# Kernel optimization log

Hardware: AMD Instinct MI355X
Metric: run time of the kernel (lower is better)

The kernel has to match this reference:

```python
import jax, jax.numpy as jnp
import numpy as np

N, E, IN, OUT, R, B = 20000, 640000, 128, 128, 64, 16


def setup_inputs() -> dict:
    key = jax.random.key(0)
    ks = jax.random.split(key, 9)
    xav_w = float(np.sqrt(2.0 / (IN + OUT)))  # xavier-uniform-ish scale
    xav_c = float(np.sqrt(2.0 / (R + B)))
    return {
        "x": jax.random.normal(ks[0], (N, IN), jnp.float32),
        "weight": jax.random.normal(ks[1], (B, IN, OUT), jnp.float32) * xav_w,
        "w_comp": jax.random.normal(ks[2], (R, B), jnp.float32) * xav_c,
        "h_bias": jnp.zeros((OUT,), jnp.float32),
        "loop_weight": jax.random.normal(ks[3], (IN, OUT), jnp.float32) * xav_w,
        "norm": jax.random.uniform(ks[4], (E, 1), jnp.float32),
        "src": jax.random.randint(ks[5], (E,), 0, N, jnp.int32),
        "dst": jax.random.randint(ks[6], (E,), 0, N, jnp.int32),
        "etypes": jax.random.randint(ks[7], (E,), 0, R, jnp.int32),
    }


def reference(x, weight, w_comp, h_bias, loop_weight, norm, src, dst, etypes):
    # Basis composition: per-relation weights W_rel[r] = sum_b w_comp[r,b] * weight[b]
    W_rel = jnp.einsum("rb,bio->rio", w_comp, weight)          # [R, IN, OUT]
    # Project every node through every relation weight (N*R << per-edge bmm
    # of E gathered [IN,OUT] matrices; same math as bmm_maybe_select).
    h_all = jnp.einsum("ni,rio->nro", x, W_rel)                 # [N, R, OUT]
    # Per-edge message: msg_e = x[src_e] @ W_rel[etype_e], scaled by norm
    msg = h_all[src, etypes] * norm                              # [E, OUT]
    # fn.sum aggregation to destination nodes
    agg = jax.ops.segment_sum(msg, dst, num_segments=x.shape[0])  # [N, OUT]
    out = agg + h_bias + x @ loop_weight                          # bias + self-loop
    return jax.nn.relu(out)                                       # activation; dropout p=0
```

## Files before the change

### kernel.cpp

```cpp
#include <hip/hip_runtime.h>

#define N_NODES 20000
#define E_EDGES 640000
#define R_REL   64
#define B_BASES 16
#define NSEG    128
#define SEGLEN  (E_EDGES / NSEG)
#define RH      10000
#define NBPR    32
#define QG      ((2 * NSEG) / 16)

typedef __attribute__((ext_vector_type(4))) float f32x4;
typedef __attribute__((ext_vector_type(8))) _Float16 half8;

__device__ inline float h2f(unsigned short v) {
    _Float16 h; __builtin_memcpy(&h, &v, 2); return (float)h;
}
__device__ inline unsigned short f2h(float f) {
    _Float16 h = (_Float16)f; unsigned short v; __builtin_memcpy(&v, &h, 2); return v;
}

__device__ inline void gld_lds16(const void* g, void* l) {
    __builtin_amdgcn_global_load_lds(
        (const __attribute__((address_space(1))) void*)g,
        (__attribute__((address_space(3))) void*)l, 16, 0, 0);
}


__global__ void k_wrelh(const float* weight, const float* w_comp, unsigned short* wt_h,
                        const float* lw, unsigned short* lwT)
{
    __shared__ float tile[32][33];
    __shared__ float wcS[B_BASES];
    int bid = blockIdx.x;
    int tx = threadIdx.x & 31, ty = threadIdx.x >> 5;
    if (bid >= R_REL * 16) {
        int q = bid - R_REL * 16;
        int ti = q >> 2, tj = q & 3;
        const float* srcp = lw + (ti * 32) * 128 + tj * 32;
        #pragma unroll
        for (int s = 0; s < 4; s++)
            tile[ty + s * 8][tx] = srcp[(ty + s * 8) * 128 + tx];
        __syncthreads();
        unsigned short* d = lwT + (tj * 32) * 128 + ti * 32;
        #pragma unroll
        for (int s = 0; s < 4; s++)
            d[(ty + s * 8) * 128 + tx] = f2h(tile[tx][ty + s * 8]);
        return;
    }
    int r  = bid >> 4;
    int ti = (bid >> 2) & 3;
    int tj = bid & 3;
    if (threadIdx.x < B_BASES) wcS[threadIdx.x] = w_comp[r * B_BASES + threadIdx.x];
    __syncthreads();
    float acc[4] = {0.f, 0.f, 0.f, 0.f};
    const float* wp = weight + (ti * 32) * 128 + tj * 32;
    for (int b = 0; b < B_BASES; b++) {
        float c = wcS[b];
        #pragma unroll
        for (int s = 0; s < 4; s++)
            acc[s] += c * wp[b * 16384 + (ty + s * 8) * 128 + tx];
    }
    #pragma unroll
    for (int s = 0; s < 4; s++) tile[ty + s * 8][tx] = acc[s];
    __syncthreads();
    unsigned short* dstp = wt_h + r * 16384 + (tj * 32) * 128 + ti * 32;
    #pragma unroll
    for (int s = 0; s < 4; s++)
        dstp[(ty + s * 8) * 128 + tx] = f2h(tile[tx][ty + s * 8]);
}

__global__ void k_xhalf(const float* x, unsigned short* xh)
{
    int i4 = blockIdx.x * 256 + threadIdx.x;
    float4 v = ((const float4*)x)[i4];
    ushort4 o;
    o.x = f2h(v.x); o.y = f2h(v.y); o.z = f2h(v.z); o.w = f2h(v.w);
    ((ushort4*)xh)[i4] = o;
}

__global__ void k_histp(const int* etypes, const int* dst, int* hp, int* he)
{
    __shared__ int lh[RH];
    __shared__ int heL[R_REL];
    int t = threadIdx.x, q = blockIdx.x;
    int s = q >> 1, h = q & 1;
    for (int i = t; i < RH; i += 256) lh[i] = 0;
    if (t < R_REL) heL[t] = 0;
    __syncthreads();
    int e0 = s * SEGLEN;
    for (int k = t; k < SEGLEN; k += 256) {
        int e = e0 + k;
        int d = dst[e];
        unsigned ld = (unsigned)(d - h * RH);
        if (ld < RH) {
            atomicAdd(&lh[ld], 1);
            atomicAdd(&heL[etypes[e]], 1);
        }
    }
    __syncthreads();
    for (int i = t; i < RH; i += 256) hp[s * N_NODES + h * RH + i] = lh[i];
    if (t < R_REL) he[q * 64 + t] = heL[t];
}

__global__ void k_sumc(const int* hp, int* counts2)
{
    int n = blockIdx.x * 256 + threadIdx.x;
    if (n >= N_NODES) return;
    int s = 0;
    for (int q = 0; q < NSEG; q += 8) {
        int v[8];
        #pragma unroll
        for (int k = 0; k < 8; k++) v[k] = hp[(q + k) * N_NODES + n];
        #pragma unroll
        for (int k = 0; k < 8; k++) s += v[k];
    }
    counts2[n] = s;
}

__global__ void k_scan_all2(const int* he, const int* counts2,
                            int* offsets, int* off2, int* be)
{
    __shared__ int part[1024];
    __shared__ int psum[16][R_REL];
    __shared__ int offL[R_REL];
    int tid = threadIdx.x;
    int t = tid & 63;
    int g = tid >> 6;
    int vals[QG];
    int ps = 0;
    #pragma unroll
    for (int k = 0; k < QG; k++) {
        vals[k] = he[(g * QG + k) * 64 + t];
        ps += vals[k];
    }
    psum[g][t] = ps;
    __syncthreads();
    if (tid < 64) {
        int c = 0;
        #pragma unroll
        for (int gg = 0; gg < 16; gg++) c += psum[gg][t];
        int s1 = c;
        for (int d = 1; d < 64; d <<= 1) {
            int a1 = __shfl_up(s1, d);
            if (t >= d) s1 += a1;
        }
        offsets[t] = s1 - c;
        offL[t] = s1 - c;
        if (t == 63) offsets[64] = s1;
    }
    __syncthreads();
    {
        int run = offL[t];
        for (int gg = 0; gg < g; gg++) run += psum[gg][t];
        #pragma unroll
        for (int k = 0; k < QG; k++) {
            be[(g * QG + k) * 64 + t] = run;
            run += vals[k];
        }
    }
    int lo_i = tid * 20, hi_i = lo_i + 20;
    if (hi_i > N_NODES) hi_i = N_NODES;
    if (lo_i > N_NODES) lo_i = N_NODES;
    int s = 0;
    for (int i = lo_i; i < hi_i; i++) s += counts2[i];
    part[tid] = s;
    __syncthreads();
    for (int d = 1; d < 1024; d <<= 1) {
        int v = (tid >= d) ? part[tid - d] : 0;
        __syncthreads();
        part[tid] += v;
        __syncthreads();
    }
    int run = part[tid] - s;
    for (int i = lo_i; i < hi_i; i++) {
        off2[i] = run;
        run += counts2[i];
    }
    if (tid == 1023) off2[N_NODES] = run;
}

__global__ void k_segbase(const int* off2, int* hp)
{
    int n = blockIdx.x * 256 + threadIdx.x;
    if (n >= N_NODES) return;
    int run = off2[n];
    for (int q = 0; q < NSEG; q += 8) {
        int v[8];
        #pragma unroll
        for (int k = 0; k < 8; k++) v[k] = hp[(q + k) * N_NODES + n];
        #pragma unroll
        for (int k = 0; k < 8; k++) { hp[(q + k) * N_NODES + n] = run; run += v[k]; }
    }
}

__global__ void k_scatter3(const int* etypes, const int* dst, const int* src, const float* norm,
                           const int* hp, const int* be,
                           int* perm_src, float* pnorm, int* pos2)
{
    __shared__ int lbase[RH];
    __shared__ int ebase[R_REL];
    int t = threadIdx.x, q = blockIdx.x;
    int s = q >> 1, h = q & 1;
    for (int i = t; i < RH; i += 256) lbase[i] = hp[s * N_NODES + h * RH + i];
    if (t < R_REL) ebase[t] = be[q * 64 + t];
    __syncthreads();
    int e0 = s * SEGLEN;
    for (int k = t; k < SEGLEN; k += 256) {
        int e = e0 + k;
        int d = dst[e];
        unsigned ld = (unsigned)(d - h * RH);
        if (ld < RH) {
            int slot = atomicAdd(&lbase[ld], 1);
            int p = atomicAdd(&ebase[etypes[e]], 1);
            perm_src[p] = src[e];
            pnorm[p] = norm[e];
            pos2[p] = slot;
        }
    }
}

__global__ __launch_bounds__(256) void k_edge_mfma(
    const unsigned short* __restrict__ xh, const unsigned short* __restrict__ wt_h,
    const int* __restrict__ perm_src, const float* __restrict__ pnorm,
    const int* __restrict__ pos2, const int* __restrict__ offsets,
    unsigned short* __restrict__ msg)
{
    __shared__ __align__(16) char smemW[32768];
    int t = threadIdx.x, b = blockIdx.x;
    int r = b >> 5;
    int j = b & (NBPR - 1);
    int p0 = offsets[r], p1 = offsets[r + 1];
    int nch = (p1 - p0 + 63) >> 6;

    {
        const size_t rbase = (size_t)r * 16384;
        #pragma unroll
        for (int it = 0; it < 8; it++) {
            int s = it * 256 + t;
            int o = s >> 4, ch = s & 15;
            int jx = ch ^ (o & 15);
            gld_lds16(wt_h + rbase + o * 128 + jx * 8, smemW + s * 16);
        }
    }

    int l = t & 63, w = t >> 6;
    int lg = l >> 4, lr = l & 15;
    int rowA = w * 16 + lr;
    const half8* smW = (const half8*)smemW;

    int i = j;
    int sN = 0;
    if (i < nch) {
        int e0 = p0 + i * 64;
        int cnt = p1 - e0; if (cnt > 64) cnt = 64;
        sN = (rowA < cnt) ? perm_src[e0 + rowA] : 0;
    }

    __syncthreads();

    half8 avC[4];
    {
        const half8* xr = (const half8*)(xh + (size_t)sN * 128);
        #pragma unroll
        for (int kk = 0; kk < 4; kk++) avC[kk] = xr[kk * 4 + lg];
    }
    int i2 = i + NBPR;
    if (i2 < nch) {
        int e0 = p0 + i2 * 64;
        int cnt = p1 - e0; if (cnt > 64) cnt = 64;
        sN = (rowA < cnt) ? perm_src[e0 + rowA] : 0;
    }

    while (i < nch) {
        int e0 = p0 + i * 64;
        int cnt = p1 - e0; if (cnt > 64) cnt = 64;

        int slotC[4]; float nrmC[4];
        #pragma unroll
        for (int jj = 0; jj < 4; jj++) {
            int row = w * 16 + lg * 4 + jj;
            bool vld = row < cnt;
            slotC[jj] = vld ? pos2[e0 + row] : -1;
            nrmC[jj]  = vld ? pnorm[e0 + row] : 0.0f;
        }

        half8 avN[4];
        {
            const half8* xr = (const half8*)(xh + (size_t)sN * 128);
            #pragma unroll
            for (int kk = 0; kk < 4; kk++) avN[kk] = xr[kk * 4 + lg];
        }
        int i3 = i2 + NBPR;
        if (i3 < nch) {
            int e0n = p0 + i3 * 64;
            int cntn = p1 - e0n; if (cntn > 64) cntn = 64;
            sN = (rowA < cntn) ? perm_src[e0n + rowA] : 0;
        }

        f32x4 acc[8];
        #pragma unroll
        for (int n = 0; n < 8; n++) acc[n] = {0.0f, 0.0f, 0.0f, 0.0f};

        #pragma unroll
        for (int kk = 0; kk < 4; kk++) {
            #pragma unroll
            for (int n = 0; n < 8; n++) {
                int o = n * 16 + lr;
                half8 bv = smW[o * 16 + ((kk * 4 + lg) ^ (o & 15))];
                acc[n] = __builtin_amdgcn_mfma_f32_16x16x32_f16(avC[kk], bv, acc[n], 0, 0, 0);
            }
        }

        #pragma unroll
        for (int jj = 0; jj < 4; jj++) {
            int slot = slotC[jj];
            if (slot >= 0) {
                float nm = nrmC[jj];
                uint4 ov;
                ov.x = (unsigned int)f2h(acc[0][jj] * nm) | ((unsigned int)f2h(acc[1][jj] * nm) << 16);
                ov.y = (unsigned int)f2h(acc[2][jj] * nm) | ((unsigned int)f2h(acc[3][jj] * nm) << 16);
                ov.z = (unsigned int)f2h(acc[4][jj] * nm) | ((unsigned int)f2h(acc[5][jj] * nm) << 16);
                ov.w = (unsigned int)f2h(acc[6][jj] * nm) | ((unsigned int)f2h(acc[7][jj] * nm) << 16);
                *(uint4*)(msg + (size_t)slot * 128 + lr * 8) = ov;
            }
        }

        #pragma unroll
        for (int kk = 0; kk < 4; kk++) avC[kk] = avN[kk];
        i = i2; i2 = i3;
    }
}

__global__ __launch_bounds__(256) void k_selfmfma(
    const unsigned short* __restrict__ xh, const unsigned short* __restrict__ lwT,
    float* __restrict__ out)
{
    __shared__ __align__(16) char smemW[32768];
    int t = threadIdx.x, b = blockIdx.x;
    int n0 = b * 64;

    #pragma unroll
    for (int it = 0; it < 8; it++) {
        int s = it * 256 + t;
        int o = s >> 4, ch = s & 15;
        int jx = ch ^ (o & 15);
        gld_lds16(lwT + o * 128 + jx * 8, smemW + s * 16);
    }

    int l = t & 63, w = t >> 6;
    int lg = l >> 4, lr = l & 15;
    int rowA = w * 16 + lr;
    int nA = n0 + rowA; if (nA >= N_NODES) nA = N_NODES - 1;
    const half8* xr = (const half8*)(xh + (size_t)nA * 128);
    half8 avC[4];
    #pragma unroll
    for (int kk = 0; kk < 4; kk++) avC[kk] = xr[kk * 4 + lg];

    f32x4 acc[8];
    #pragma unroll
    for (int n = 0; n < 8; n++) acc[n] = {0.0f, 0.0f, 0.0f, 0.0f};

    __syncthreads();

    const half8* smW = (const half8*)smemW;
    #pragma unroll
    for (int kk = 0; kk < 4; kk++) {
        #pragma unroll
        for (int n = 0; n < 8; n++) {
            int o = n * 16 + lr;
            half8 bv = smW[o * 16 + ((kk * 4 + lg) ^ (o & 15))];
            acc[n] = __builtin_amdgcn_mfma_f32_16x16x32_f16(avC[kk], bv, acc[n], 0, 0, 0);
        }
    }

    #pragma unroll
    for (int jj = 0; jj < 4; jj++) {
        int row = w * 16 + lg * 4 + jj;
        int n = n0 + row;
        if (n < N_NODES) {
            float4 v0, v1;
            v0.x = acc[0][jj]; v0.y = acc[1][jj]; v0.z = acc[2][jj]; v0.w = acc[3][jj];
            v1.x = acc[4][jj]; v1.y = acc[5][jj]; v1.z = acc[6][jj]; v1.w = acc[7][jj];
            *(float4*)(out + (size_t)n * 128 + lr * 8) = v0;
            *(float4*)(out + (size_t)n * 128 + lr * 8 + 4) = v1;
        }
    }
}

__global__ void k_msgsum(const unsigned short* msg, const int* off2,
                         const float* bias, float* out)
{
    __shared__ float4 red[256];
    __shared__ float fin[128];
    int n = blockIdx.x, t = threadIdx.x;
    int m0 = off2[n], m1 = off2[n + 1];
    int rp = t >> 5, c = t & 31;
    float4 a; a.x = 0.f; a.y = 0.f; a.z = 0.f; a.w = 0.f;
    for (int j = m0 + rp; j < m1; j += 8) {
        uint2 v = *(const uint2*)(msg + (size_t)j * 128 + c * 4);
        a.x += h2f((unsigned short)(v.x & 0xffff));
        a.y += h2f((unsigned short)(v.x >> 16));
        a.z += h2f((unsigned short)(v.y & 0xffff));
        a.w += h2f((unsigned short)(v.y >> 16));
    }
    red[t] = a;
    __syncthreads();
    if (t < 128) {
        float4 b = red[t + 128];
        red[t].x += b.x; red[t].y += b.y; red[t].z += b.z; red[t].w += b.w;
    }
    __syncthreads();
    if (t < 64) {
        float4 b = red[t + 64];
        red[t].x += b.x; red[t].y += b.y; red[t].z += b.z; red[t].w += b.w;
    }
    __syncthreads();
    if (t < 32) {
        float4 v = red[t], b = red[t + 32];
        v.x += b.x; v.y += b.y; v.z += b.z; v.w += b.w;
        float4 o = *(const float4*)(out + (size_t)n * 128 + t * 4);
        v.x += o.x; v.y += o.y; v.z += o.z; v.w += o.w;
        int base = (t & 1) * 64 + (t >> 1);
        fin[base]      = v.x;
        fin[base + 16] = v.y;
        fin[base + 32] = v.z;
        fin[base + 48] = v.w;
    }
    __syncthreads();
    if (t < 32) {
        float4 f = ((const float4*)fin)[t];
        float4 bb = *(const float4*)(bias + t * 4);
        f.x += bb.x; f.y += bb.y; f.z += bb.z; f.w += bb.w;
        if (f.x < 0.f) f.x = 0.f;
        if (f.y < 0.f) f.y = 0.f;
        if (f.z < 0.f) f.z = 0.f;
        if (f.w < 0.f) f.w = 0.f;
        *(float4*)(out + (size_t)n * 128 + t * 4) = f;
    }
}


__global__ void k_wrel(const float* weight, const float* w_comp, float* W_rel)
{
    int idx = blockIdx.x * 256 + threadIdx.x;
    int r  = idx >> 14;
    int io = idx & 16383;
    float acc = 0.0f;
    for (int b = 0; b < B_BASES; b++)
        acc += w_comp[r * B_BASES + b] * weight[b * 16384 + io];
    W_rel[idx] = acc;
}

__global__ void k_zero(float* agg, int* counts, int* counts2)
{
    int idx = blockIdx.x * 256 + threadIdx.x;
    if (idx < N_NODES * 128) agg[idx] = 0.0f;
    if (idx < R_REL) counts[idx] = 0;
    if (idx < N_NODES) counts2[idx] = 0;
}

__global__ void k_hist(const int* etypes, int* counts)
{
    __shared__ int h[R_REL];
    int t = threadIdx.x;
    if (t < R_REL) h[t] = 0;
    __syncthreads();
    int e = blockIdx.x * 256 + t;
    atomicAdd(&h[etypes[e]], 1);
    __syncthreads();
    if (t < R_REL && h[t] != 0) atomicAdd(&counts[t], h[t]);
}

__global__ void k_scan(const int* counts, int* offsets, int* cursor, int* co)
{
    if (threadIdx.x == 0) {
        int run = 0, c = 0;
        for (int r = 0; r < R_REL; r++) {
            offsets[r] = run; cursor[r] = run; co[r] = c;
            run += counts[r];
            c   += (counts[r] + 63) >> 6;
        }
        offsets[R_REL] = run; co[R_REL] = c;
    }
}

__global__ void k_scatter(const int* etypes, int* cursor, int* perm)
{
    __shared__ int h[R_REL];
    __shared__ int base[R_REL];
    int t = threadIdx.x;
    if (t < R_REL) h[t] = 0;
    __syncthreads();
    int e = blockIdx.x * 256 + t;
    int et = etypes[e];
    int rank = atomicAdd(&h[et], 1);
    __syncthreads();
    if (t < R_REL && h[t] != 0) base[t] = atomicAdd(&cursor[t], h[t]);
    __syncthreads();
    perm[base[et] + rank] = e;
}

__global__ void k_edge_atomic(const float* x, const float* W_rel, const float* norm,
                              const int* src, const int* dst, const int* perm,
                              const int* offsets, const int* co, float* agg)
{
    __shared__ float4 WfS[2048];
    __shared__ float4 xsS[1024];
    __shared__ int coS[R_REL + 1];
    __shared__ int srcS[64], dstS[64];
    __shared__ float normS[64];
    int t = threadIdx.x, bid = blockIdx.x;
    if (t <= R_REL) coS[t] = co[t];
    __syncthreads();
    if (bid >= coS[R_REL]) return;
    int r = 0;
    while (bid >= coS[r + 1]) r++;
    int e0 = offsets[r] + (bid - coS[r]) * 64;
    int cnt = offsets[r + 1] - e0;
    if (cnt > 64) cnt = 64;
    if (t < 64) {
        if (t < cnt) {
            int eid = perm[e0 + t];
            srcS[t] = src[eid]; dstS[t] = dst[eid]; normS[t] = norm[eid];
        } else { srcS[t] = 0; dstS[t] = 0; normS[t] = 0.0f; }
    }
    const float* xsf = (const float*)xsS;
    int q  = t & 31;
    int eb = t >> 5;
    float4 acc[8];
    for (int k = 0; k < 8; k++) { acc[k].x = 0.f; acc[k].y = 0.f; acc[k].z = 0.f; acc[k].w = 0.f; }
    for (int h = 0; h < 2; h++) {
        __syncthreads();
        const float4* Wsrc = (const float4*)(W_rel + r * 16384 + h * 8192);
        for (int p = 0; p < 8; p++) WfS[p * 256 + t] = Wsrc[p * 256 + t];
        for (int p = 0; p < 4; p++) {
            int idx = p * 256 + t;
            int e = idx >> 4, c = idx & 15;
            xsS[idx] = ((const float4*)(x + srcS[e] * 128 + h * 64))[c];
        }
        __syncthreads();
        for (int i = 0; i < 64; i++) {
            float4 wv = WfS[i * 32 + q];
            for (int k = 0; k < 8; k++) {
                float xv = xsf[(eb + 8 * k) * 64 + i];
                acc[k].x += xv * wv.x;
                acc[k].y += xv * wv.y;
                acc[k].z += xv * wv.z;
                acc[k].w += xv * wv.w;
            }
        }
    }
    for (int k = 0; k < 8; k++) {
        int e = eb + 8 * k;
        if (e < cnt) {
            float nrm = normS[e];
            float* row = agg + dstS[e] * 128 + q * 4;
            atomicAdd(row + 0, acc[k].x * nrm);
            atomicAdd(row + 1, acc[k].y * nrm);
            atomicAdd(row + 2, acc[k].z * nrm);
            atomicAdd(row + 3, acc[k].w * nrm);
        }
    }
}

__global__ void k_out(const float* x, const float* loop_w, const float* agg,
                      const float* bias, float* out)
{
    __shared__ float xrow[128];
    int n = blockIdx.x;
    int o = threadIdx.x;
    xrow[o] = x[n * 128 + o];
    __syncthreads();
    float acc = 0.0f;
    for (int i = 0; i < 128; i++)
        acc += xrow[i] * loop_w[i * 128 + o];
    float val = acc + agg[n * 128 + o] + bias[o];
    if (val < 0.0f) val = 0.0f;
    out[n * 128 + o] = val;
}

extern "C" void kernel_launch(void* const* d_in, const int* in_sizes, int n_in,
                              void* d_out, int out_size, void* d_ws, size_t ws_size,
                              hipStream_t stream)
{
    const float* x      = (const float*)d_in[0];
    const float* weight = (const float*)d_in[1];
    const float* w_comp = (const float*)d_in[2];
    const float* h_bias = (const float*)d_in[3];
    const float* loop_w = (const float*)d_in[4];
    const float* norm   = (const float*)d_in[5];
    const int* src    = (const int*)d_in[6];
    const int* dst    = (const int*)d_in[7];
    const int* etypes = (const int*)d_in[8];
    float* out = (float*)d_out;

    char* ws = (char*)d_ws;
    size_t off = 0;
    float* W_rel = (float*)(ws + off); off += (size_t)R_REL * 16384 * 4;
    float* agg   = (float*)(ws + off); off += (size_t)N_NODES * 128 * 4;
    int* perm    = (int*)(ws + off);   off += (size_t)E_EDGES * 4;
    int* counts  = (int*)(ws + off);   off += 64 * 4;
    int* offsets = (int*)(ws + off);   off += 68 * 4;
    int* cursor  = (int*)(ws + off);   off += 64 * 4;
    int* co      = (int*)(ws + off);   off += 68 * 4;
    int* counts2 = (int*)(ws + off);   off += (size_t)N_NODES * 4;
    int* off2    = (int*)(ws + off);   off += (size_t)(N_NODES + 4) * 4;
    int* cursor2 = (int*)(ws + off);   off += (size_t)N_NODES * 4;
    int* pos2    = (int*)(ws + off);   off += (size_t)E_EDGES * 4;
    unsigned short* msg = (unsigned short*)(ws + off);
    size_t need_big = off + (size_t)E_EDGES * 128 * 2;
    int big = (ws_size >= need_big) ? 1 : 0;

    if (big) {
        unsigned short* wt_h = (unsigned short*)W_rel;
        char* wspare = (char*)W_rel + (size_t)2 * 1024 * 1024;
        unsigned short* lwT = (unsigned short*)wspare;
        unsigned short* xh = (unsigned short*)agg;
        float* pnorm = (float*)((char*)agg + (size_t)N_NODES * 128 * 2);
        int* perm_src = perm;
        int* hp = (int*)msg;
        int* he = (int*)((char*)msg + (size_t)NSEG * N_NODES * 4);
        int* be = (int*)((char*)he + (size_t)2 * NSEG * 64 * 4);

        k_wrelh<<<R_REL * 16 + 16, 256, 0, stream>>>(weight, w_comp, wt_h, loop_w, lwT);
        k_xhalf<<<(N_NODES * 128 / 4) / 256, 256, 0, stream>>>(x, xh);
        k_histp<<<2 * NSEG, 256, 0, stream>>>(etypes, dst, hp, he);
        k_sumc<<<(N_NODES + 255) / 256, 256, 0, stream>>>(hp, counts2);
        k_scan_all2<<<1, 1024, 0, stream>>>(he, counts2, offsets, off2, be);
        k_segbase<<<(N_NODES + 255) / 256, 256, 0, stream>>>(off2, hp);
        k_scatter3<<<2 * NSEG, 256, 0, stream>>>(etypes, dst, src, norm,
                                                 hp, be, perm_src, pnorm, pos2);
        k_edge_mfma<<<R_REL * NBPR, 256, 0, stream>>>(
            xh, wt_h, perm_src, pnorm, pos2, offsets, msg);
        k_selfmfma<<<(N_NODES + 63) / 64, 256, 0, stream>>>(xh, lwT, out);
        k_msgsum<<<N_NODES, 256, 0, stream>>>(msg, off2, h_bias, out);
    } else {
        k_wrel<<<(R_REL * 16384) / 256, 256, 0, stream>>>(weight, w_comp, W_rel);
        k_zero<<<(N_NODES * 128) / 256, 256, 0, stream>>>(agg, counts, counts2);
        k_hist<<<E_EDGES / 256, 256, 0, stream>>>(etypes, counts);
        k_scan<<<1, 64, 0, stream>>>(counts, offsets, cursor, co);
        k_scatter<<<E_EDGES / 256, 256, 0, stream>>>(etypes, cursor, perm);
        k_edge_atomic<<<E_EDGES / 64 + R_REL, 256, 0, stream>>>(
            x, W_rel, norm, src, dst, perm, offsets, co, agg);
        k_out<<<N_NODES, 128, 0, stream>>>(x, loop_w, agg, h_bias, out);
    }
}
```

Before: 266.4 us.

## Merge prep kernels, compress per-segment histograms to u16, fuse self-loop into edge kernel

Merges the weight composition, loop-weight transpose, x-to-half conversion and histogram kernels into one launch. Per-segment node histograms are stored as 16-bit values, and k_segbase now computes segment-local prefixes without off2, which k_scatter3 adds back. The self-loop MFMA blocks are appended to the edge-MFMA grid. The intent is fewer launches and less histogram traffic. It relies on a single segment's count per node fitting in 16 bits, and it makes the block roles in the merged grids uneven.

Result: no change. 268.7 us (+0.8%).

```diff
diff --git a/kernel.cpp b/kernel.cpp
--- a/kernel.cpp
+++ b/kernel.cpp
@@ -10,6 +10,13 @@
 #define NBPR    32
 #define QG      ((2 * NSEG) / 16)
 
+#define PB_WREL (R_REL * 16)
+#define PB_LW   (PB_WREL + 16)
+#define PB_XH   (PB_LW + 2500)
+#define PB_HIST (PB_XH + 2 * NSEG)
+
+#define SELF_B  ((N_NODES + 63) / 64)
+
 typedef __attribute__((ext_vector_type(4))) float f32x4;
 typedef __attribute__((ext_vector_type(8))) _Float16 half8;
 
@@ -26,16 +33,44 @@
         (__attribute__((address_space(3))) void*)l, 16, 0, 0);
 }
 
-
-__global__ void k_wrelh(const float* weight, const float* w_comp, unsigned short* wt_h,
-                        const float* lw, unsigned short* lwT)
+__global__ void k_prep(const float* weight, const float* w_comp, unsigned short* wt_h,
+                       const float* lw, unsigned short* lwT,
+                       const float* x, unsigned short* xh,
+                       const int* etypes, const int* dst,
+                       unsigned short* hps, int* he)
 {
     __shared__ float tile[32][33];
     __shared__ float wcS[B_BASES];
-    int bid = blockIdx.x;
-    int tx = threadIdx.x & 31, ty = threadIdx.x >> 5;
-    if (bid >= R_REL * 16) {
-        int q = bid - R_REL * 16;
+    __shared__ int lh[RH];
+    __shared__ int heL[R_REL];
+    int b = blockIdx.x, t = threadIdx.x;
+    int tx = t & 31, ty = t >> 5;
+
+    if (b < PB_WREL) {
+        int r  = b >> 4;
+        int ti = (b >> 2) & 3;
+        int tj = b & 3;
+        if (t < B_BASES) wcS[t] = w_comp[r * B_BASES + t];
+        __syncthreads();
+        float acc[4] = {0.f, 0.f, 0.f, 0.f};
+        const float* wp = weight + (ti * 32) * 128 + tj * 32;
+        for (int bb = 0; bb < B_BASES; bb++) {
+            float c = wcS[bb];
+            #pragma unroll
+            for (int s = 0; s < 4; s++)
+                acc[s] += c * wp[bb * 16384 + (ty + s * 8) * 128 + tx];
+        }
+        #pragma unroll
+        for (int s = 0; s < 4; s++) tile[ty + s * 8][tx] = acc[s];
+        __syncthreads();
+        unsigned short* dstp = wt_h + r * 16384 + (tj * 32) * 128 + ti * 32;
+        #pragma unroll
+        for (int s = 0; s < 4; s++)
+            dstp[(ty + s * 8) * 128 + tx] = f2h(tile[tx][ty + s * 8]);
+        return;
+    }
+    if (b < PB_LW) {
+        int q = b - PB_WREL;
         int ti = q >> 2, tj = q & 3;
         const float* srcp = lw + (ti * 32) * 128 + tj * 32;
         #pragma unroll
@@ -48,62 +83,38 @@
             d[(ty + s * 8) * 128 + tx] = f2h(tile[tx][ty + s * 8]);
         return;
     }
-    int r  = bid >> 4;
-    int ti = (bid >> 2) & 3;
-    int tj = bid & 3;
-    if (threadIdx.x < B_BASES) wcS[threadIdx.x] = w_comp[r * B_BASES + threadIdx.x];
-    __syncthreads();
-    float acc[4] = {0.f, 0.f, 0.f, 0.f};
-    const float* wp = weight + (ti * 32) * 128 + tj * 32;
-    for (int b = 0; b < B_BASES; b++) {
-        float c = wcS[b];
-        #pragma unroll
-        for (int s = 0; s < 4; s++)
-            acc[s] += c * wp[b * 16384 + (ty + s * 8) * 128 + tx];
-    }
-    #pragma unroll
-    for (int s = 0; s < 4; s++) tile[ty + s * 8][tx] = acc[s];
-    __syncthreads();
-    unsigned short* dstp = wt_h + r * 16384 + (tj * 32) * 128 + ti * 32;
-    #pragma unroll
-    for (int s = 0; s < 4; s++)
-        dstp[(ty + s * 8) * 128 + tx] = f2h(tile[tx][ty + s * 8]);
-}
-
-__global__ void k_xhalf(const float* x, unsigned short* xh)
-{
-    int i4 = blockIdx.x * 256 + threadIdx.x;
-    float4 v = ((const float4*)x)[i4];
-    ushort4 o;
-    o.x = f2h(v.x); o.y = f2h(v.y); o.z = f2h(v.z); o.w = f2h(v.w);
-    ((ushort4*)xh)[i4] = o;
-}
-
-__global__ void k_histp(const int* etypes, const int* dst, int* hp, int* he)
-{
-    __shared__ int lh[RH];
-    __shared__ int heL[R_REL];
-    int t = threadIdx.x, q = blockIdx.x;
-    int s = q >> 1, h = q & 1;
-    for (int i = t; i < RH; i += 256) lh[i] = 0;
-    if (t < R_REL) heL[t] = 0;
-    __syncthreads();
-    int e0 = s * SEGLEN;
-    for (int k = t; k < SEGLEN; k += 256) {
-        int e = e0 + k;
-        int d = dst[e];
-        unsigned ld = (unsigned)(d - h * RH);
-        if (ld < RH) {
-            atomicAdd(&lh[ld], 1);
-            atomicAdd(&heL[etypes[e]], 1);
-        }
-    }
-    __syncthreads();
-    for (int i = t; i < RH; i += 256) hp[s * N_NODES + h * RH + i] = lh[i];
-    if (t < R_REL) he[q * 64 + t] = heL[t];
-}
-
-__global__ void k_sumc(const int* hp, int* counts2)
+    if (b < PB_XH) {
+        int i4 = (b - PB_LW) * 256 + t;
+        float4 v = ((const float4*)x)[i4];
+        ushort4 o;
+        o.x = f2h(v.x); o.y = f2h(v.y); o.z = f2h(v.z); o.w = f2h(v.w);
+        ((ushort4*)xh)[i4] = o;
+        return;
+    }
+    {
+        int q = b - PB_XH;
+        int s = q >> 1, h = q & 1;
+        for (int i = t; i < RH; i += 256) lh[i] = 0;
+        if (t < R_REL) heL[t] = 0;
+        __syncthreads();
+        int e0 = s * SEGLEN;
+        for (int k = t; k < SEGLEN; k += 256) {
+            int e = e0 + k;
+            int d = dst[e];
+            unsigned ld = (unsigned)(d - h * RH);
+            if (ld < RH) {
+                atomicAdd(&lh[ld], 1);
+                atomicAdd(&heL[etypes[e]], 1);
+            }
+        }
+        __syncthreads();
+        for (int i = t; i < RH; i += 256)
+            hps[(size_t)s * N_NODES + h * RH + i] = (unsigned short)lh[i];
+        if (t < R_REL) he[q * 64 + t] = heL[t];
+    }
+}
+
+__global__ void k_sumc(const unsigned short* hps, int* counts2)
 {
     int n = blockIdx.x * 256 + threadIdx.x;
     if (n >= N_NODES) return;
@@ -111,11 +122,28 @@
     for (int q = 0; q < NSEG; q += 8) {
         int v[8];
         #pragma unroll
-        for (int k = 0; k < 8; k++) v[k] = hp[(q + k) * N_NODES + n];
+        for (int k = 0; k < 8; k++) v[k] = hps[(size_t)(q + k) * N_NODES + n];
         #pragma unroll
         for (int k = 0; k < 8; k++) s += v[k];
     }
     counts2[n] = s;
+}
+
+__global__ void k_segbase(unsigned short* hps)
+{
+    int n = blockIdx.x * 256 + threadIdx.x;
+    if (n >= N_NODES) return;
+    int run = 0;
+    for (int q = 0; q < NSEG; q += 8) {
+        int v[8];
+        #pragma unroll
+        for (int k = 0; k < 8; k++) v[k] = hps[(size_t)(q + k) * N_NODES + n];
+        #pragma unroll
+        for (int k = 0; k < 8; k++) {
+            hps[(size_t)(q + k) * N_NODES + n] = (unsigned short)run;
+            run += v[k];
+        }
+    }
 }
 
 __global__ void k_scan_all2(const int* he, const int* counts2,
@@ -180,29 +208,16 @@
     if (tid == 1023) off2[N_NODES] = run;
 }
 
-__global__ void k_segbase(const int* off2, int* hp)
-{
-    int n = blockIdx.x * 256 + threadIdx.x;
-    if (n >= N_NODES) return;
-    int run = off2[n];
-    for (int q = 0; q < NSEG; q += 8) {
-        int v[8];
-        #pragma unroll
-        for (int k = 0; k < 8; k++) v[k] = hp[(q + k) * N_NODES + n];
-        #pragma unroll
-        for (int k = 0; k < 8; k++) { hp[(q + k) * N_NODES + n] = run; run += v[k]; }
-    }
-}
-
 __global__ void k_scatter3(const int* etypes, const int* dst, const int* src, const float* norm,
-                           const int* hp, const int* be,
+                           const unsigned short* hps, const int* be, const int* off2,
                            int* perm_src, float* pnorm, int* pos2)
 {
     __shared__ int lbase[RH];
     __shared__ int ebase[R_REL];
     int t = threadIdx.x, q = blockIdx.x;
     int s = q >> 1, h = q & 1;
-    for (int i = t; i < RH; i += 256) lbase[i] = hp[s * N_NODES + h * RH + i];
+    for (int i = t; i < RH; i += 256)
+        lbase[i] = off2[h * RH + i] + (int)hps[(size_t)s * N_NODES + h * RH + i];
     if (t < R_REL) ebase[t] = be[q * 64 + t];
     __syncthreads();
     int e0 = s * SEGLEN;
@@ -222,12 +237,60 @@
 
 __global__ __launch_bounds__(256) void k_edge_mfma(
     const unsigned short* __restrict__ xh, const unsigned short* __restrict__ wt_h,
+    const unsigned short* __restrict__ lwT,
     const int* __restrict__ perm_src, const float* __restrict__ pnorm,
     const int* __restrict__ pos2, const int* __restrict__ offsets,
-    unsigned short* __restrict__ msg)
+    unsigned short* __restrict__ msg, float* __restrict__ out)
 {
     __shared__ __align__(16) char smemW[32768];
     int t = threadIdx.x, b = blockIdx.x;
+    int l = t & 63, w = t >> 6;
+    int lg = l >> 4, lr = l & 15;
+    const half8* smW = (const half8*)smemW;
+
+    if (b >= R_REL * NBPR) {
+        int n0 = (b - R_REL * NBPR) * 64;
+        #pragma unroll
+        for (int it = 0; it < 8; it++) {
+            int s = it * 256 + t;
+            int o = s >> 4, ch = s & 15;
+            int jx = ch ^ (o & 15);
+            gld_lds16(lwT + o * 128 + jx * 8, smemW + s * 16);
+        }
+        int rowA = w * 16 + lr;
+        int nA = n0 + rowA; if (nA >= N_NODES) nA = N_NODES - 1;
+        const half8* xr = (const half8*)(xh + (size_t)nA * 128);
+        half8 avC[4];
+        #pragma unroll
+        for (int kk = 0; kk < 4; kk++) avC[kk] = xr[kk * 4 + lg];
+        f32x4 acc[8];
+        #pragma unroll
+        for (int n = 0; n < 8; n++) acc[n] = {0.0f, 0.0f, 0.0f, 0.0f};
+        __syncthreads();
+        #pragma unroll
+        for (int kk = 0; kk < 4; kk++) {
+            #pragma unroll
+            for (int n = 0; n < 8; n++) {
+                int o = n * 16 + lr;
+                half8 bv = smW[o * 16 + ((kk * 4 + lg) ^ (o & 15))];
+                acc[n] = __builtin_amdgcn_mfma_f32_16x16x32_f16(avC[kk], bv, acc[n], 0, 0, 0);
+            }
+        }
+        #pragma unroll
+        for (int jj = 0; jj < 4; jj++) {
+            int row = w * 16 + lg * 4 + jj;
+            int n = n0 + row;
+            if (n < N_NODES) {
+                float4 v0, v1;
+                v0.x = acc[0][jj]; v0.y = acc[1][jj]; v0.z = acc[2][jj]; v0.w = acc[3][jj];
+                v1.x = acc[4][jj]; v1.y = acc[5][jj]; v1.z = acc[6][jj]; v1.w = acc[7][jj];
+                *(float4*)(out + (size_t)n * 128 + lr * 8) = v0;
+                *(float4*)(out + (size_t)n * 128 + lr * 8 + 4) = v1;
+            }
+        }
+        return;
+    }
+
     int r = b >> 5;
     int j = b & (NBPR - 1);
     int p0 = offsets[r], p1 = offsets[r + 1];
@@ -244,10 +307,7 @@
         }
     }
 
-    int l = t & 63, w = t >> 6;
-    int lg = l >> 4, lr = l & 15;
     int rowA = w * 16 + lr;
-    const half8* smW = (const half8*)smemW;
 
     int i = j;
     int sN = 0;
@@ -329,62 +389,6 @@
         #pragma unroll
         for (int kk = 0; kk < 4; kk++) avC[kk] = avN[kk];
         i = i2; i2 = i3;
-    }
-}
-
-__global__ __launch_bounds__(256) void k_selfmfma(
-    const unsigned short* __restrict__ xh, const unsigned short* __restrict__ lwT,
-    float* __restrict__ out)
-{
-    __shared__ __align__(16) char smemW[32768];
-    int t = threadIdx.x, b = blockIdx.x;
-    int n0 = b * 64;
-
-    #pragma unroll
-    for (int it = 0; it < 8; it++) {
-        int s = it * 256 + t;
-        int o = s >> 4, ch = s & 15;
-        int jx = ch ^ (o & 15);
-        gld_lds16(lwT + o * 128 + jx * 8, smemW + s * 16);
-    }
-
-    int l = t & 63, w = t >> 6;
-    int lg = l >> 4, lr = l & 15;
-    int rowA = w * 16 + lr;
-    int nA = n0 + rowA; if (nA >= N_NODES) nA = N_NODES - 1;
-    const half8* xr = (const half8*)(xh + (size_t)nA * 128);
-    half8 avC[4];
-    #pragma unroll
-    for (int kk = 0; kk < 4; kk++) avC[kk] = xr[kk * 4 + lg];
-
-    f32x4 acc[8];
-    #pragma unroll
-    for (int n = 0; n < 8; n++) acc[n] = {0.0f, 0.0f, 0.0f, 0.0f};
-
-    __syncthreads();
-
-    const half8* smW = (const half8*)smemW;
-    #pragma unroll
-    for (int kk = 0; kk < 4; kk++) {
-        #pragma unroll
-        for (int n = 0; n < 8; n++) {
-            int o = n * 16 + lr;
-            half8 bv = smW[o * 16 + ((kk * 4 + lg) ^ (o & 15))];
-            acc[n] = __builtin_amdgcn_mfma_f32_16x16x32_f16(avC[kk], bv, acc[n], 0, 0, 0);
-        }
-    }
-
-    #pragma unroll
-    for (int jj = 0; jj < 4; jj++) {
-        int row = w * 16 + lg * 4 + jj;
-        int n = n0 + row;
-        if (n < N_NODES) {
-            float4 v0, v1;
-            v0.x = acc[0][jj]; v0.y = acc[1][jj]; v0.z = acc[2][jj]; v0.w = acc[3][jj];
-            v1.x = acc[4][jj]; v1.y = acc[5][jj]; v1.z = acc[6][jj]; v1.w = acc[7][jj];
-            *(float4*)(out + (size_t)n * 128 + lr * 8) = v0;
-            *(float4*)(out + (size_t)n * 128 + lr * 8 + 4) = v1;
-        }
     }
 }
 
@@ -619,21 +623,19 @@
         unsigned short* xh = (unsigned short*)agg;
         float* pnorm = (float*)((char*)agg + (size_t)N_NODES * 128 * 2);
         int* perm_src = perm;
-        int* hp = (int*)msg;
-        int* he = (int*)((char*)msg + (size_t)NSEG * N_NODES * 4);
+        unsigned short* hps = (unsigned short*)msg;
+        int* he = (int*)((char*)msg + (size_t)NSEG * N_NODES * 2);
         int* be = (int*)((char*)he + (size_t)2 * NSEG * 64 * 4);
 
-        k_wrelh<<<R_REL * 16 + 16, 256, 0, stream>>>(weight, w_comp, wt_h, loop_w, lwT);
-        k_xhalf<<<(N_NODES * 128 / 4) / 256, 256, 0, stream>>>(x, xh);
-        k_histp<<<2 * NSEG, 256, 0, stream>>>(etypes, dst, hp, he);
-        k_sumc<<<(N_NODES + 255) / 256, 256, 0, stream>>>(hp, counts2);
+        k_prep<<<PB_HIST, 256, 0, stream>>>(weight, w_comp, wt_h, loop_w, lwT,
+                                            x, xh, etypes, dst, hps, he);
+        k_sumc<<<(N_NODES + 255) / 256, 256, 0, stream>>>(hps, counts2);
+        k_segbase<<<(N_NODES + 255) / 256, 256, 0, stream>>>(hps);
         k_scan_all2<<<1, 1024, 0, stream>>>(he, counts2, offsets, off2, be);
-        k_segbase<<<(N_NODES + 255) / 256, 256, 0, stream>>>(off2, hp);
         k_scatter3<<<2 * NSEG, 256, 0, stream>>>(etypes, dst, src, norm,
-                                                 hp, be, perm_src, pnorm, pos2);
-        k_edge_mfma<<<R_REL * NBPR, 256, 0, stream>>>(
-            xh, wt_h, perm_src, pnorm, pos2, offsets, msg);
-        k_selfmfma<<<(N_NODES + 63) / 64, 256, 0, stream>>>(xh, lwT, out);
+                                                 hps, be, off2, perm_src, pnorm, pos2);
+        k_edge_mfma<<<R_REL * NBPR + SELF_B, 256, 0, stream>>>(
+            xh, wt_h, lwT, perm_src, pnorm, pos2, offsets, msg, out);
         k_msgsum<<<N_NODES, 256, 0, stream>>>(msg, off2, h_bias, out);
     } else {
         k_wrel<<<(R_REL * 16384) / 256, 256, 0, stream>>>(weight, w_comp, W_rel);
```
